# Optimization experiments

Measured on AMD Instinct MI355X. Metric: run time of the kernel, lower is better.

The kernel has to match this reference:

```python
import jax, jax.numpy as jnp
import numpy as np

N_EMBED = 1024
NUM_EXPERTS = 8
TOP_K = 2
D_FF = 4 * N_EMBED
B, S = 4, 2048


def setup_inputs() -> dict:
    key = jax.random.key(0)
    ks = jax.random.split(key, 8)
    s = 0.02
    return {
        "x": jax.random.normal(ks[0], (B, S, N_EMBED), jnp.float32),
        "noise": jax.random.normal(ks[1], (B, S, NUM_EXPERTS), jnp.float32),
        "w_route": jax.random.normal(ks[2], (N_EMBED, NUM_EXPERTS), jnp.float32) * s,
        "b_route": jnp.zeros((NUM_EXPERTS,), jnp.float32),
        "w_noise": jax.random.normal(ks[3], (N_EMBED, NUM_EXPERTS), jnp.float32) * s,
        "b_noise": jnp.zeros((NUM_EXPERTS,), jnp.float32),
        "w1": jax.random.normal(ks[4], (NUM_EXPERTS, N_EMBED, D_FF), jnp.float32) * s,
        "b1": jnp.zeros((NUM_EXPERTS, D_FF), jnp.float32),
        "w2": jax.random.normal(ks[5], (NUM_EXPERTS, D_FF, N_EMBED), jnp.float32) * s,
        "b2": jnp.zeros((NUM_EXPERTS, N_EMBED), jnp.float32),
    }


def reference(x, noise, w_route, b_route, w_noise, b_noise, w1, b1, w2, b2):
    # NoisyTopkRouter: logits + N(0,1)*softplus(noise_logits), top-k, softmax
    # over a sparse (-inf filled) logit matrix -> gates are exactly 0 for
    # non-selected experts.
    logits = x @ w_route + b_route                                   # [B,S,E]
    noise_logits = x @ w_noise + b_noise                             # [B,S,E]
    noisy = logits + noise * jax.nn.softplus(noise_logits)           # [B,S,E]
    _, topi = jax.lax.top_k(noisy, TOP_K)                            # [B,S,k]
    sel = jax.nn.one_hot(topi, NUM_EXPERTS, dtype=bool).any(-2)      # [B,S,E]
    sparse_logits = jnp.where(sel, noisy, -jnp.inf)
    gates = jax.nn.softmax(sparse_logits, axis=-1)                   # [B,S,E]

    T = x.shape[0] * x.shape[1]
    xf = x.reshape(T, N_EMBED)                                       # [T,d]
    gf = gates.reshape(T, NUM_EXPERTS)                               # [T,E]

    # Dense per-expert MLP weighted by gates; gate==0 for unselected tokens,
    # so this matches the masked gather/scatter of the original exactly.
    out = jnp.zeros_like(xf)
    for e in range(NUM_EXPERTS):
        h = jax.nn.relu(xf @ w1[e] + b1[e])                          # [T,4d]
        y = h @ w2[e] + b2[e]                                        # [T,d]
        out = out + y * gf[:, e:e + 1]
    return out.reshape(x.shape)
```

## Files before the change

### kernel.cpp

```cpp
#include <hip/hip_runtime.h>

typedef __bf16 bf16_t;
typedef __bf16 bf16x8 __attribute__((ext_vector_type(8)));
typedef __bf16 bf16x4 __attribute__((ext_vector_type(4)));
typedef __bf16 bf16x2 __attribute__((ext_vector_type(2)));
typedef float  f32x4  __attribute__((ext_vector_type(4)));
typedef unsigned int u32;
typedef u32 u32x4 __attribute__((ext_vector_type(4)));

#define T_TOK 8192
#define DIM   1024
#define DFF   4096
#define NEXP  8

__device__ __forceinline__ void gll16(const void* g, void* l) {
    __builtin_amdgcn_global_load_lds(
        (const __attribute__((address_space(1))) char*)g,
        (__attribute__((address_space(3))) char*)l, 16, 0, 0);
}

__device__ __forceinline__ void transpose_tile(
    const float* __restrict__ src, bf16_t* __restrict__ dst,
    int R, int C, int r0, int c0, int tid, u32* lds)
{
    {
        int cg = tid & 15, rp = tid >> 4;
#pragma unroll
        for (int i = 0; i < 2; ++i) {
            int p = rp + i * 16;
            f32x4 a = *(const f32x4*)&src[(size_t)(r0 + 2 * p) * C + c0 + cg * 4];
            f32x4 b = *(const f32x4*)&src[(size_t)(r0 + 2 * p + 1) * C + c0 + cg * 4];
#pragma unroll
            for (int j = 0; j < 4; ++j) {
                int c = cg * 4 + j;
                union { bf16x2 h; u32 w; } cv;
                cv.h[0] = (bf16_t)a[j];
                cv.h[1] = (bf16_t)b[j];
                int ps = p ^ (((c >> 2) & 7) << 2);
                lds[c * 32 + ps] = cv.w;
            }
        }
    }
    __syncthreads();
    {
        int q = tid & 7, ccb = tid >> 3;
#pragma unroll
        for (int i = 0; i < 2; ++i) {
            int cc = ccb + i * 32;
            int ps = (q * 4) ^ ((((cc) >> 2) & 7) << 2);
            u32x4 v = *(const u32x4*)&lds[cc * 32 + ps];
            *(u32x4*)&dst[(size_t)(c0 + cc) * R + r0 + q * 8] = v;
        }
    }
}

__global__ __launch_bounds__(256) void fused_pre_kernel(
    const float* __restrict__ x, const float* __restrict__ noise,
    const float* __restrict__ w_route, const float* __restrict__ b_route,
    const float* __restrict__ w_noise, const float* __restrict__ b_noise,
    const float* __restrict__ w1, const float* __restrict__ w2,
    bf16_t* __restrict__ w1t, bf16_t* __restrict__ w2t,
    int* __restrict__ counts, int* __restrict__ lists, float* __restrict__ gate_tok)
{
    __shared__ u32 lds[64 * 32];
    int id = blockIdx.x;
    int tid = threadIdx.x;

    if (id >= 2048) {
        if (id < 10240) {
            int t1 = id - 2048;
            int e = t1 >> 10, rem = t1 & 1023;
            int bx = rem & 63, by = rem >> 6;
            transpose_tile(w1 + (size_t)e * DIM * DFF, w1t + (size_t)e * DIM * DFF,
                           DIM, DFF, by * 64, bx * 64, tid, lds);
        } else {
            int t2 = id - 10240;
            int e = t2 >> 10, rem = t2 & 1023;
            int bx = rem & 15, by = rem >> 4;
            transpose_tile(w2 + (size_t)e * DFF * DIM, w2t + (size_t)e * DFF * DIM,
                           DFF, DIM, by * 64, bx * 64, tid, lds);
        }
        return;
    }

    int wave = tid >> 6;
    int lane = tid & 63;
    int tok = id * 4 + wave;
    if (tok >= T_TOK) return;

    const float* xr = x + (size_t)tok * DIM;
    double aR[NEXP], aN[NEXP];
#pragma unroll
    for (int e = 0; e < NEXP; ++e) { aR[e] = 0.0; aN[e] = 0.0; }

#pragma unroll 4
    for (int i = 0; i < 16; ++i) {
        int k = lane + i * 64;
        double xv = (double)xr[k];
        const float4* wr4 = (const float4*)(w_route + (size_t)k * 8);
        const float4* wn4 = (const float4*)(w_noise + (size_t)k * 8);
        float4 r0 = wr4[0], r1 = wr4[1];
        float4 n0 = wn4[0], n1 = wn4[1];
        aR[0] += xv * (double)r0.x; aR[1] += xv * (double)r0.y;
        aR[2] += xv * (double)r0.z; aR[3] += xv * (double)r0.w;
        aR[4] += xv * (double)r1.x; aR[5] += xv * (double)r1.y;
        aR[6] += xv * (double)r1.z; aR[7] += xv * (double)r1.w;
        aN[0] += xv * (double)n0.x; aN[1] += xv * (double)n0.y;
        aN[2] += xv * (double)n0.z; aN[3] += xv * (double)n0.w;
        aN[4] += xv * (double)n1.x; aN[5] += xv * (double)n1.y;
        aN[6] += xv * (double)n1.z; aN[7] += xv * (double)n1.w;
    }
#pragma unroll
    for (int e = 0; e < NEXP; ++e) {
        for (int s = 1; s < 64; s <<= 1) {
            aR[e] += __shfl_xor(aR[e], s);
            aN[e] += __shfl_xor(aN[e], s);
        }
    }
    if (lane == 0) {
        double nv[NEXP];
#pragma unroll
        for (int e = 0; e < NEXP; ++e) {
            double lg = aR[e] + (double)b_route[e];
            double nl = aN[e] + (double)b_noise[e];
            double sp = (nl > 30.0) ? nl : log1p(exp(nl));
            nv[e] = lg + (double)noise[(size_t)tok * 8 + e] * sp;
        }
        int i1 = 0;
#pragma unroll
        for (int e = 1; e < NEXP; ++e) if (nv[e] > nv[i1]) i1 = e;
        int i2 = (i1 == 0) ? 1 : 0;
#pragma unroll
        for (int e = 0; e < NEXP; ++e) if (e != i1 && nv[e] > nv[i2]) i2 = e;
        double m = nv[i1];
        double e2 = exp(nv[i2] - m);
        double s = 1.0 + e2;
        gate_tok[2 * tok + 0] = (float)(1.0 / s);
        gate_tok[2 * tok + 1] = (float)(e2 / s);
        int p1 = atomicAdd(&counts[i1], 1);
        lists[i1 * T_TOK + p1] = 2 * tok + 0;
        int p2 = atomicAdd(&counts[i2], 1);
        lists[i2 * T_TOK + p2] = 2 * tok + 1;
    }
}

__global__ void prefix_kernel(const int* __restrict__ counts, int* __restrict__ bases) {
    if (threadIdx.x == 0 && blockIdx.x == 0) {
        int s = 0;
#pragma unroll
        for (int e = 0; e < NEXP; ++e) { bases[e] = s; s += counts[e]; }
    }
}

__global__ __launch_bounds__(256) void pack_a_kernel(
    const float* __restrict__ x, const int* __restrict__ bases,
    const int* __restrict__ lists, bf16_t* __restrict__ Ap, int* __restrict__ inv)
{
    int wave = threadIdx.x >> 6, lane = threadIdx.x & 63;
    int p = blockIdx.x * 4 + wave;
    int e = 0;
#pragma unroll
    for (int i = 1; i < NEXP; ++i) e += (p >= bases[i]);
    int pos = p - bases[e];
    int entry = lists[e * T_TOK + pos];
    if (lane == 0) inv[entry] = p;
    const f32x4* src = (const f32x4*)(x + (size_t)(entry >> 1) * DIM);
    bf16x8* dst = (bf16x8*)(Ap + (size_t)p * DIM);
#pragma unroll
    for (int j = 0; j < 2; ++j) {
        int c = lane + j * 64;
        f32x4 a = src[c * 2 + 0];
        f32x4 b = src[c * 2 + 1];
        bf16x8 o;
        o[0] = (bf16_t)a[0]; o[1] = (bf16_t)a[1]; o[2] = (bf16_t)a[2]; o[3] = (bf16_t)a[3];
        o[4] = (bf16_t)b[0]; o[5] = (bf16_t)b[1]; o[6] = (bf16_t)b[2]; o[7] = (bf16_t)b[3];
        dst[c] = o;
    }
}

template<int K, int MODE>
__global__ __launch_bounds__(256) void moe_gemm_kernel(
    const bf16_t* __restrict__ Asrc, const bf16_t* __restrict__ Wt,
    const float* __restrict__ bias,
    const int* __restrict__ counts, const int* __restrict__ bases,
    const int* __restrict__ lists, const float* __restrict__ gate_tok,
    bf16_t* __restrict__ Hout, bf16_t* __restrict__ Yp)
{
    constexpr int N = (MODE == 0) ? DFF : DIM;
    constexpr int NT = K / 64;
    constexpr int NY = N / 128;

    int wg = blockIdx.x + 64 * (blockIdx.y + NY * blockIdx.z);
    int e = wg & 7;
    int inner = wg >> 3;
    int xi = inner & 63;
    int yi = inner >> 6;

    int cnt = counts[e];
    int m0 = xi * 128;
    if (m0 >= cnt) return;
    int base = bases[e];
    int n0 = yi * 128;
    const int* list = lists + e * T_TOK;
    const bf16_t* W = Wt + (size_t)e * N * K;

    __shared__ __attribute__((aligned(16))) bf16_t Ah0[128 * 64];
    __shared__ __attribute__((aligned(16))) bf16_t Bh0[128 * 64];
    __shared__ __attribute__((aligned(16))) bf16_t Ah1[128 * 64];
    __shared__ __attribute__((aligned(16))) bf16_t Bh1[128 * 64];

    int tid = threadIdx.x;
    int lane = tid & 63;
    int wave = tid >> 6;
    int wr = wave >> 1, wc = wave & 1;

    int kcs = (((lane & 7) ^ (lane >> 3)) << 3);
    const bf16_t* pA[4];
    const bf16_t* pB[4];
#pragma unroll
    for (int i = 0; i < 4; ++i) {
        int c = wave * 4 + i;
        int r = c * 8 + (lane >> 3);
        int ridx = m0 + r; if (ridx > cnt - 1) ridx = cnt - 1;
        pA[i] = Asrc + (size_t)(base + ridx) * K + kcs;
        pB[i] = W + (size_t)(n0 + r) * K + kcs;
    }

    f32x4 acc[4][4];
#pragma unroll
    for (int m = 0; m < 4; ++m)
#pragma unroll
        for (int n = 0; n < 4; ++n)
            acc[m][n] = (f32x4){0.f, 0.f, 0.f, 0.f};

    int g = lane >> 4, ln15 = lane & 15, ln7 = lane & 7;

#define STAGE(An, Bn, k0) do {                                               \
    _Pragma("unroll") for (int i = 0; i < 4; ++i) {                          \
        int c = wave * 4 + i;                                                \
        gll16(pA[i] + (k0), (An) + c * 512);                                 \
        gll16(pB[i] + (k0), (Bn) + c * 512);                                 \
    } } while (0)

#define COMPUTE(Ab, Bb) do {                                                 \
    _Pragma("unroll") for (int kk = 0; kk < 2; ++kk) {                       \
        bf16x8 a[4], b[4];                                                   \
        int sw = (((kk * 4 + g) ^ ln7) << 3);                                \
        _Pragma("unroll") for (int n = 0; n < 4; ++n)                        \
            b[n] = *(const bf16x8*)((Bb) + (wc * 64 + n * 16 + ln15) * 64 + sw); \
        _Pragma("unroll") for (int m = 0; m < 4; ++m)                        \
            a[m] = *(const bf16x8*)((Ab) + (wr * 64 + m * 16 + ln15) * 64 + sw); \
        __builtin_amdgcn_s_setprio(1);                                       \
        _Pragma("unroll") for (int m = 0; m < 4; ++m)                        \
            _Pragma("unroll") for (int n = 0; n < 4; ++n)                    \
                acc[m][n] = __builtin_amdgcn_mfma_f32_16x16x32_bf16(a[m], b[n], acc[m][n], 0, 0, 0); \
        __builtin_amdgcn_s_setprio(0);                                       \
    } } while (0)

#define FENCE() __builtin_amdgcn_sched_barrier(0)
#define WAITV(n) asm volatile("s_waitcnt vmcnt(" #n ")" ::: "memory")

    STAGE(Ah0, Bh0, 0);

    for (int kt = 0; kt < NT; kt += 2) {
        if (kt + 1 < NT) { STAGE(Ah1, Bh1, (kt + 1) * 64); WAITV(8); }
        else             { WAITV(0); }
        FENCE(); __builtin_amdgcn_s_barrier(); FENCE();
        COMPUTE(Ah0, Bh0);
        FENCE(); __builtin_amdgcn_s_barrier(); FENCE();
        if (kt + 2 < NT) { STAGE(Ah0, Bh0, (kt + 2) * 64); WAITV(8); }
        else             { WAITV(0); }
        FENCE(); __builtin_amdgcn_s_barrier(); FENCE();
        COMPUTE(Ah1, Bh1);
        FENCE(); __builtin_amdgcn_s_barrier(); FENCE();
    }
#undef STAGE
#undef COMPUTE
#undef FENCE
#undef WAITV

    int l4 = lane >> 4;
    float bs[4];
#pragma unroll
    for (int n = 0; n < 4; ++n)
        bs[n] = bias[e * N + n0 + wc * 64 + n * 16 + ln15];
#pragma unroll
    for (int m = 0; m < 4; ++m) {
#pragma unroll
        for (int j = 0; j < 4; ++j) {
            int grow = m0 + wr * 64 + m * 16 + l4 * 4 + j;
            if (grow >= cnt) continue;
            if constexpr (MODE == 0) {
#pragma unroll
                for (int n = 0; n < 4; ++n) {
                    int gcol = n0 + wc * 64 + n * 16 + ln15;
                    float v = acc[m][n][j] + bs[n];
                    Hout[(size_t)(base + grow) * DFF + gcol] = (bf16_t)fmaxf(v, 0.f);
                }
            } else {
                float gt = gate_tok[list[grow]];
#pragma unroll
                for (int n = 0; n < 4; ++n) {
                    int gcol = n0 + wc * 64 + n * 16 + ln15;
                    Yp[(size_t)(base + grow) * DIM + gcol] = (bf16_t)(gt * (acc[m][n][j] + bs[n]));
                }
            }
        }
    }
}

__global__ __launch_bounds__(256) void combine_kernel(
    const bf16_t* __restrict__ Yp, const int* __restrict__ inv,
    float* __restrict__ out)
{
    int q = threadIdx.x >> 7, i = threadIdx.x & 127;
    int t = blockIdx.x * 2 + q;
    int p0 = inv[2 * t], p1 = inv[2 * t + 1];
    bf16x8 va = ((const bf16x8*)(Yp + (size_t)p0 * DIM))[i];
    bf16x8 vb = ((const bf16x8*)(Yp + (size_t)p1 * DIM))[i];
    f32x4 o0, o1;
#pragma unroll
    for (int j = 0; j < 4; ++j) {
        o0[j] = (float)va[j] + (float)vb[j];
        o1[j] = (float)va[4 + j] + (float)vb[4 + j];
    }
    f32x4* o = (f32x4*)(out + (size_t)t * DIM + i * 8);
    o[0] = o0;
    o[1] = o1;
}

extern "C" void kernel_launch(void* const* d_in, const int* in_sizes, int n_in,
                              void* d_out, int out_size, void* d_ws, size_t ws_size,
                              hipStream_t stream) {
    const float* x       = (const float*)d_in[0];
    const float* noise   = (const float*)d_in[1];
    const float* w_route = (const float*)d_in[2];
    const float* b_route = (const float*)d_in[3];
    const float* w_noise = (const float*)d_in[4];
    const float* b_noise = (const float*)d_in[5];
    const float* w1      = (const float*)d_in[6];
    const float* b1      = (const float*)d_in[7];
    const float* w2      = (const float*)d_in[8];
    const float* b2      = (const float*)d_in[9];
    float* out = (float*)d_out;

    char* ws = (char*)d_ws;
    size_t off = 0;
    auto alloc = [&](size_t bytes) {
        off = (off + 255) & ~(size_t)255;
        size_t r = off; off += bytes; return r;
    };
    int*    counts   = (int*)   (ws + alloc(32));
    int*    bases    = (int*)   (ws + alloc(32));
    int*    lists    = (int*)   (ws + alloc((size_t)NEXP * T_TOK * 4));
    float*  gate_tok = (float*) (ws + alloc((size_t)T_TOK * 2 * 4));
    int*    inv      = (int*)   (ws + alloc((size_t)T_TOK * 2 * 4));
    bf16_t* w1t      = (bf16_t*)(ws + alloc((size_t)NEXP * DFF * DIM * 2));
    bf16_t* w2t      = (bf16_t*)(ws + alloc((size_t)NEXP * DIM * DFF * 2));
    bf16_t* Ap       = (bf16_t*)(ws + alloc((size_t)T_TOK * 2 * DIM * 2));
    bf16_t* H        = (bf16_t*)(ws + alloc((size_t)T_TOK * 2 * DFF * 2));
    bf16_t* Yp       = w1t;
    (void)ws_size; (void)in_sizes; (void)n_in; (void)out_size;

    hipMemsetAsync(counts, 0, 32, stream);

    fused_pre_kernel<<<18432, 256, 0, stream>>>(x, noise, w_route, b_route, w_noise, b_noise,
                                                w1, w2, w1t, w2t, counts, lists, gate_tok);

    prefix_kernel<<<1, 64, 0, stream>>>(counts, bases);
    pack_a_kernel<<<T_TOK * 2 / 4, 256, 0, stream>>>(x, bases, lists, Ap, inv);

    moe_gemm_kernel<DIM, 0><<<dim3(64, DFF / 128, NEXP), 256, 0, stream>>>(
        Ap, w1t, b1, counts, bases, lists, gate_tok, H, nullptr);
    moe_gemm_kernel<DFF, 1><<<dim3(64, DIM / 128, NEXP), 256, 0, stream>>>(
        H, w2t, b2, counts, bases, lists, gate_tok, nullptr, Yp);

    combine_kernel<<<T_TOK / 2, 256, 0, stream>>>(Yp, inv, out);
}
```

Baseline: 742.9 us.

## Fold x bf16 cast into pre kernel and gather rows inside first GEMM

Drops the prefix and pack kernels. The pre kernel now also casts x to bf16 once per token, and the first expert GEMM reads A rows indirectly through the expert token list instead of from a packed buffer. Expert base offsets are recomputed from counts inside the GEMM and combine kernels, and inv now stores an (expert, position) pair. This removes two launches and a duplicated 2x pack write. The cost is an indirect, non-contiguous row gather in GEMM1's A loads.

```diff
diff --git a/kernel.cpp b/kernel.cpp
--- a/kernel.cpp
+++ b/kernel.cpp
@@ -59,22 +59,23 @@
     const float* __restrict__ w_route, const float* __restrict__ b_route,
     const float* __restrict__ w_noise, const float* __restrict__ b_noise,
     const float* __restrict__ w1, const float* __restrict__ w2,
-    bf16_t* __restrict__ w1t, bf16_t* __restrict__ w2t,
-    int* __restrict__ counts, int* __restrict__ lists, float* __restrict__ gate_tok)
+    bf16_t* __restrict__ w1t, bf16_t* __restrict__ w2t, bf16_t* __restrict__ xb,
+    int* __restrict__ counts, int* __restrict__ lists, float* __restrict__ gate_tok,
+    int* __restrict__ inv)
 {
     __shared__ u32 lds[64 * 32];
     int id = blockIdx.x;
     int tid = threadIdx.x;
 
-    if (id >= 2048) {
-        if (id < 10240) {
-            int t1 = id - 2048;
+    if (id >= 4096) {
+        if (id < 12288) {
+            int t1 = id - 4096;
             int e = t1 >> 10, rem = t1 & 1023;
             int bx = rem & 63, by = rem >> 6;
             transpose_tile(w1 + (size_t)e * DIM * DFF, w1t + (size_t)e * DIM * DFF,
                            DIM, DFF, by * 64, bx * 64, tid, lds);
         } else {
-            int t2 = id - 10240;
+            int t2 = id - 12288;
             int e = t2 >> 10, rem = t2 & 1023;
             int bx = rem & 15, by = rem >> 4;
             transpose_tile(w2 + (size_t)e * DFF * DIM, w2t + (size_t)e * DFF * DIM,
@@ -85,6 +86,24 @@
 
     int wave = tid >> 6;
     int lane = tid & 63;
+
+    if (id >= 2048) {
+        int tok = (id - 2048) * 4 + wave;
+        const f32x4* src = (const f32x4*)(x + (size_t)tok * DIM);
+        bf16x8* dst = (bf16x8*)(xb + (size_t)tok * DIM);
+#pragma unroll
+        for (int j = 0; j < 2; ++j) {
+            int c = lane + j * 64;
+            f32x4 a = src[c * 2 + 0];
+            f32x4 b = src[c * 2 + 1];
+            bf16x8 o;
+            o[0] = (bf16_t)a[0]; o[1] = (bf16_t)a[1]; o[2] = (bf16_t)a[2]; o[3] = (bf16_t)a[3];
+            o[4] = (bf16_t)b[0]; o[5] = (bf16_t)b[1]; o[6] = (bf16_t)b[2]; o[7] = (bf16_t)b[3];
+            dst[c] = o;
+        }
+        return;
+    }
+
     int tok = id * 4 + wave;
     if (tok >= T_TOK) return;
 
@@ -139,42 +158,10 @@
         gate_tok[2 * tok + 1] = (float)(e2 / s);
         int p1 = atomicAdd(&counts[i1], 1);
         lists[i1 * T_TOK + p1] = 2 * tok + 0;
+        inv[2 * tok + 0] = (i1 << 13) | p1;
         int p2 = atomicAdd(&counts[i2], 1);
         lists[i2 * T_TOK + p2] = 2 * tok + 1;
-    }
-}
-
-__global__ void prefix_kernel(const int* __restrict__ counts, int* __restrict__ bases) {
-    if (threadIdx.x == 0 && blockIdx.x == 0) {
-        int s = 0;
-#pragma unroll
-        for (int e = 0; e < NEXP; ++e) { bases[e] = s; s += counts[e]; }
-    }
-}
-
-__global__ __launch_bounds__(256) void pack_a_kernel(
-    const float* __restrict__ x, const int* __restrict__ bases,
-    const int* __restrict__ lists, bf16_t* __restrict__ Ap, int* __restrict__ inv)
-{
-    int wave = threadIdx.x >> 6, lane = threadIdx.x & 63;
-    int p = blockIdx.x * 4 + wave;
-    int e = 0;
-#pragma unroll
-    for (int i = 1; i < NEXP; ++i) e += (p >= bases[i]);
-    int pos = p - bases[e];
-    int entry = lists[e * T_TOK + pos];
-    if (lane == 0) inv[entry] = p;
-    const f32x4* src = (const f32x4*)(x + (size_t)(entry >> 1) * DIM);
-    bf16x8* dst = (bf16x8*)(Ap + (size_t)p * DIM);
-#pragma unroll
-    for (int j = 0; j < 2; ++j) {
-        int c = lane + j * 64;
-        f32x4 a = src[c * 2 + 0];
-        f32x4 b = src[c * 2 + 1];
-        bf16x8 o;
-        o[0] = (bf16_t)a[0]; o[1] = (bf16_t)a[1]; o[2] = (bf16_t)a[2]; o[3] = (bf16_t)a[3];
-        o[4] = (bf16_t)b[0]; o[5] = (bf16_t)b[1]; o[6] = (bf16_t)b[2]; o[7] = (bf16_t)b[3];
-        dst[c] = o;
+        inv[2 * tok + 1] = (i2 << 13) | p2;
     }
 }
 
@@ -182,8 +169,8 @@
 __global__ __launch_bounds__(256) void moe_gemm_kernel(
     const bf16_t* __restrict__ Asrc, const bf16_t* __restrict__ Wt,
     const float* __restrict__ bias,
-    const int* __restrict__ counts, const int* __restrict__ bases,
-    const int* __restrict__ lists, const float* __restrict__ gate_tok,
+    const int* __restrict__ counts, const int* __restrict__ lists,
+    const float* __restrict__ gate_tok,
     bf16_t* __restrict__ Hout, bf16_t* __restrict__ Yp)
 {
     constexpr int N = (MODE == 0) ? DFF : DIM;
@@ -196,10 +183,19 @@
     int xi = inner & 63;
     int yi = inner >> 6;
 
-    int cnt = counts[e];
+    int cnt, base;
+    {
+        int s = 0, c = 0, b = 0;
+#pragma unroll
+        for (int i = 0; i < NEXP; ++i) {
+            int ci = counts[i];
+            if (i == e) { b = s; c = ci; }
+            s += ci;
+        }
+        cnt = c; base = b;
+    }
     int m0 = xi * 128;
     if (m0 >= cnt) return;
-    int base = bases[e];
     int n0 = yi * 128;
     const int* list = lists + e * T_TOK;
     const bf16_t* W = Wt + (size_t)e * N * K;
@@ -222,7 +218,10 @@
         int c = wave * 4 + i;
         int r = c * 8 + (lane >> 3);
         int ridx = m0 + r; if (ridx > cnt - 1) ridx = cnt - 1;
-        pA[i] = Asrc + (size_t)(base + ridx) * K + kcs;
+        size_t arow;
+        if constexpr (MODE == 0) arow = (size_t)(list[ridx] >> 1);
+        else                     arow = (size_t)(base + ridx);
+        pA[i] = Asrc + arow * K + kcs;
         pB[i] = W + (size_t)(n0 + r) * K + kcs;
     }
 
@@ -311,11 +310,19 @@
 
 __global__ __launch_bounds__(256) void combine_kernel(
     const bf16_t* __restrict__ Yp, const int* __restrict__ inv,
-    float* __restrict__ out)
+    const int* __restrict__ counts, float* __restrict__ out)
 {
+    int bs[NEXP];
+    {
+        int s = 0;
+#pragma unroll
+        for (int i = 0; i < NEXP; ++i) { bs[i] = s; s += counts[i]; }
+    }
     int q = threadIdx.x >> 7, i = threadIdx.x & 127;
     int t = blockIdx.x * 2 + q;
-    int p0 = inv[2 * t], p1 = inv[2 * t + 1];
+    int v0 = inv[2 * t], v1 = inv[2 * t + 1];
+    int p0 = bs[v0 >> 13] + (v0 & 8191);
+    int p1 = bs[v1 >> 13] + (v1 & 8191);
     bf16x8 va = ((const bf16x8*)(Yp + (size_t)p0 * DIM))[i];
     bf16x8 vb = ((const bf16x8*)(Yp + (size_t)p1 * DIM))[i];
     f32x4 o0, o1;
@@ -351,29 +358,25 @@
         size_t r = off; off += bytes; return r;
     };
     int*    counts   = (int*)   (ws + alloc(32));
-    int*    bases    = (int*)   (ws + alloc(32));
     int*    lists    = (int*)   (ws + alloc((size_t)NEXP * T_TOK * 4));
     float*  gate_tok = (float*) (ws + alloc((size_t)T_TOK * 2 * 4));
     int*    inv      = (int*)   (ws + alloc((size_t)T_TOK * 2 * 4));
     bf16_t* w1t      = (bf16_t*)(ws + alloc((size_t)NEXP * DFF * DIM * 2));
     bf16_t* w2t      = (bf16_t*)(ws + alloc((size_t)NEXP * DIM * DFF * 2));
-    bf16_t* Ap       = (bf16_t*)(ws + alloc((size_t)T_TOK * 2 * DIM * 2));
+    bf16_t* xb       = (bf16_t*)(ws + alloc((size_t)T_TOK * DIM * 2));
     bf16_t* H        = (bf16_t*)(ws + alloc((size_t)T_TOK * 2 * DFF * 2));
     bf16_t* Yp       = w1t;
     (void)ws_size; (void)in_sizes; (void)n_in; (void)out_size;
 
     hipMemsetAsync(counts, 0, 32, stream);
 
-    fused_pre_kernel<<<18432, 256, 0, stream>>>(x, noise, w_route, b_route, w_noise, b_noise,
-                                                w1, w2, w1t, w2t, counts, lists, gate_tok);
-
-    prefix_kernel<<<1, 64, 0, stream>>>(counts, bases);
-    pack_a_kernel<<<T_TOK * 2 / 4, 256, 0, stream>>>(x, bases, lists, Ap, inv);
+    fused_pre_kernel<<<20480, 256, 0, stream>>>(x, noise, w_route, b_route, w_noise, b_noise,
+                                                w1, w2, w1t, w2t, xb, counts, lists, gate_tok, inv);
 
     moe_gemm_kernel<DIM, 0><<<dim3(64, DFF / 128, NEXP), 256, 0, stream>>>(
-        Ap, w1t, b1, counts, bases, lists, gate_tok, H, nullptr);
+        xb, w1t, b1, counts, lists, gate_tok, H, nullptr);
     moe_gemm_kernel<DFF, 1><<<dim3(64, DIM / 128, NEXP), 256, 0, stream>>>(
-        H, w2t, b2, counts, bases, lists, gate_tok, nullptr, Yp);
-
-    combine_kernel<<<T_TOK / 2, 256, 0, stream>>>(Yp, inv, out);
-}
+        H, w2t, b2, counts, lists, gate_tok, nullptr, Yp);
+
+    combine_kernel<<<T_TOK / 2, 256, 0, stream>>>(Yp, inv, counts, out);
+}
```

After: 737.3 us. About the same (-0.7%).
